# Kernel optimization log

Measured on AMD Instinct MI355X. Metric: run time of the kernel, lower is better.

The kernel has to match this reference:

```python
import jax, jax.numpy as jnp
import numpy as np

B, F_IN, NCH, T = 1, 1, 1536, 128
NW = [476, 476, 292]          # wires per plane (face 0)
NC = [10000, 10000, 10000]    # crossings per plane pair (01, 12, 20)
NCROSS = sum(NC)
E = 120000                    # ~4 nearest-neighbor edges per crossing node
N_FEAT_WIRE = 4
OUT_CH = 4
NODE_DIM = 2 * (F_IN + N_FEAT_WIRE) + 3  # = 13, matches GAT input dim


def setup_inputs() -> dict:
    key = jax.random.key(0)
    ks = jax.random.split(key, 18)
    x = jax.random.normal(ks[0], (B, F_IN, NCH, T), jnp.float32)
    chan_p0 = jax.random.randint(ks[1], (NW[0],), 0, NCH, jnp.int32)
    chan_p1 = jax.random.randint(ks[2], (NW[1],), 0, NCH, jnp.int32)
    chan_p2 = jax.random.randint(ks[3], (NW[2],), 0, NCH, jnp.int32)
    gidx_01 = jax.random.randint(ks[4], (NC[0], 2), 0, min(NW[0], NW[1]), jnp.int32)
    gidx_12 = jax.random.randint(ks[5], (NC[1], 2), 0, min(NW[1], NW[2]), jnp.int32)
    gidx_20 = jax.random.randint(ks[6], (NC[2], 2), 0, min(NW[2], NW[0]), jnp.int32)
    ray_01 = jax.random.normal(ks[7], (NC[0], 2), jnp.float32)
    ray_12 = jax.random.normal(ks[8], (NC[1], 2), jnp.float32)
    ray_20 = jax.random.normal(ks[9], (NC[2], 2), jnp.float32)
    edges = jax.random.randint(ks[10], (2, E), 0, NCROSS, jnp.int32)
    W_gat = jax.random.normal(ks[11], (NODE_DIM, OUT_CH), jnp.float32) * 0.1
    a_src = jax.random.normal(ks[12], (OUT_CH,), jnp.float32) * 0.1
    a_dst = jax.random.normal(ks[13], (OUT_CH,), jnp.float32) * 0.1
    b_gat = jnp.zeros((OUT_CH,), jnp.float32)
    W_mlp = jax.random.normal(ks[14], (OUT_CH, 1), jnp.float32) * 0.1
    b_mlp = jnp.zeros((1,), jnp.float32)
    return dict(x=x, chan_p0=chan_p0, chan_p1=chan_p1, chan_p2=chan_p2,
                gidx_01=gidx_01, gidx_12=gidx_12, gidx_20=gidx_20,
                ray_01=ray_01, ray_12=ray_12, ray_20=ray_20, edges=edges,
                W_gat=W_gat, a_src=a_src, a_dst=a_dst, b_gat=b_gat,
                W_mlp=W_mlp, b_mlp=b_mlp)


def _plane_feats(x, chan, plane_id):
    # x: [B,F,C,T] -> per-wire features [B,T,Nw,F+4]:
    # (signal, wire_ident, channel, 0, plane_id) -- mirrors as_wires_f0_pX.
    sig = jnp.transpose(x[:, :, chan, :], (0, 3, 2, 1))  # [B,T,Nw,F]
    nw = chan.shape[0]
    wire_id = jnp.arange(nw, dtype=jnp.float32)
    extra = jnp.stack([wire_id, chan.astype(jnp.float32),
                       jnp.zeros(nw, jnp.float32),
                       jnp.full((nw,), plane_id, jnp.float32)], axis=-1)  # [Nw,4]
    extra = jnp.broadcast_to(extra[None, None], sig.shape[:2] + extra.shape)
    return jnp.concatenate([sig, extra], axis=-1)


def _cross(fA, fB, gidx, rc):
    # crossing node features: wireA feats ++ wireB feats ++ ray xy ++ tick
    n = gidx.shape[0]
    tick = jnp.broadcast_to(jnp.arange(T, dtype=jnp.float32)[None, :, None, None],
                            (B, T, n, 1))
    rcb = jnp.broadcast_to(rc[None, None], (B, T, n, 2))
    return jnp.concatenate([fA[:, :, gidx[:, 0]], fB[:, :, gidx[:, 1]], rcb, tick],
                           axis=-1)  # [B,T,n,13]


def _gat_one(h, a_src, a_dst, src, dst):
    # single-graph, single-head GAT attention + aggregation. h: [N,OUT_CH]
    s = h @ a_src  # [N]
    d = h @ a_dst
    e = jax.nn.leaky_relu(s[src] + d[dst], 0.2)  # [E]
    m = jax.ops.segment_max(e, dst, num_segments=NCROSS)
    m = jnp.where(jnp.isfinite(m), m, 0.0)
    w = jnp.exp(e - m[dst])
    denom = jax.ops.segment_sum(w, dst, num_segments=NCROSS)
    msg = jax.ops.segment_sum(w[:, None] * h[src], dst, num_segments=NCROSS)
    return msg / (denom[:, None] + 1e-9)


def reference(x, chan_p0, chan_p1, chan_p2, gidx_01, gidx_12, gidx_20,
              ray_01, ray_12, ray_20, edges,
              W_gat, a_src, a_dst, b_gat, W_mlp, b_mlp):
    f0 = _plane_feats(x, chan_p0, 0.0)
    f1 = _plane_feats(x, chan_p1, 1.0)
    f2 = _plane_feats(x, chan_p2, 2.0)
    nodes = jnp.concatenate([_cross(f0, f1, gidx_01, ray_01),
                             _cross(f1, f2, gidx_12, ray_12),
                             _cross(f2, f0, gidx_20, ray_20)], axis=2)  # [B,T,N,13]
    h = nodes @ W_gat + b_gat  # [B,T,N,OUT_CH]
    src, dst = edges[0], edges[1]
    gat = jax.vmap(jax.vmap(lambda hh: _gat_one(hh, a_src, a_dst, src, dst)))
    g = gat(h)  # [B,T,N,OUT_CH]
    return jax.nn.sigmoid(g @ W_mlp + b_mlp)  # [B,T,N,1]
```

## Files before the change

### kernel.cpp

```cpp
#include <hip/hip_runtime.h>

#define T_TICKS 128
#define NCHAN   1536
#define NCPAIR  10000
#define NCROSS  30000
#define E_EDGES 120000
#define TG      8
#define NTG     (T_TICKS / TG)
#define NBLK_N  ((NCROSS + 255) / 256)
#define CAP     24
#define EPB     ((E_EDGES + NBLK_N - 1) / NBLK_N)


__global__ void k_feat(const float* __restrict__ x,
                       const int* __restrict__ c0, const int* __restrict__ c1,
                       const int* __restrict__ c2,
                       const int* __restrict__ g01, const int* __restrict__ g12,
                       const int* __restrict__ g20,
                       const float* __restrict__ r01,
                       const float* __restrict__ r12,
                       const float* __restrict__ r20,
                       const float* __restrict__ Wg,
                       const float* __restrict__ bg,
                       const float* __restrict__ as_,
                       const float* __restrict__ ad_,
                       const float* __restrict__ Wm,
                       const int* __restrict__ e_src,
                       const int* __restrict__ e_dst,
                       int* __restrict__ counts,
                       unsigned short* __restrict__ bucket,
                       float4* __restrict__ sp4, float4* __restrict__ dc4) {
    const int tid = threadIdx.x;
    const int tg = blockIdx.y;
    if (tg == 0) {
        const int lo = blockIdx.x * EPB;
        const int hi = min(lo + EPB, E_EDGES);
        for (int i = lo + tid; i < hi; i += 256) {
            const int s = e_src[i];
            const int d = e_dst[i];
            const int slot = atomicAdd(&counts[d], 1);
            if (slot < CAP) bucket[(size_t)d * CAP + slot] = (unsigned short)s;
        }
    }
    const int n = blockIdx.x * 256 + tid;
    if (n >= NCROSS) return;

    int iA, iB, m;
    float pA, pB;
    const int* cA;
    const int* cB;
    const float* ray;
    if (n < NCPAIR) {
        m = n; cA = c0; cB = c1; pA = 0.f; pB = 1.f; ray = r01;
        iA = g01[2 * m]; iB = g01[2 * m + 1];
    } else if (n < 2 * NCPAIR) {
        m = n - NCPAIR; cA = c1; cB = c2; pA = 1.f; pB = 2.f; ray = r12;
        iA = g12[2 * m]; iB = g12[2 * m + 1];
    } else {
        m = n - 2 * NCPAIR; cA = c2; cB = c0; pA = 2.f; pB = 0.f; ray = r20;
        iA = g20[2 * m]; iB = g20[2 * m + 1];
    }
    const int chA = cA[iA];
    const int chB = cB[iB];
    const float rx = ray[2 * m];
    const float ry = ray[2 * m + 1];

    float base[4];
#pragma unroll
    for (int c = 0; c < 4; c++) {
        base[c] = bg[c]
                + (float)iA  * Wg[1 * 4 + c] + (float)chA * Wg[2 * 4 + c]
                + pA         * Wg[4 * 4 + c]
                + (float)iB  * Wg[6 * 4 + c] + (float)chB * Wg[7 * 4 + c]
                + pB         * Wg[9 * 4 + c]
                + rx         * Wg[10 * 4 + c] + ry * Wg[11 * 4 + c];
    }
    float sB = 0, dB = 0, pBs = 0;
    float sA1 = 0, dA1 = 0, pA1 = 0;
    float sB1 = 0, dB1 = 0, pB1 = 0;
    float sT = 0, dT = 0, pT = 0;
#pragma unroll
    for (int c = 0; c < 4; c++) {
        const float va = as_[c], vd = ad_[c], vm = Wm[c];
        sB  += base[c] * va;  dB  += base[c] * vd;  pBs += base[c] * vm;
        sA1 += Wg[c] * va;    dA1 += Wg[c] * vd;    pA1 += Wg[c] * vm;
        sB1 += Wg[5*4+c]*va;  dB1 += Wg[5*4+c]*vd;  pB1 += Wg[5*4+c]*vm;
        sT  += Wg[12*4+c]*va; dT  += Wg[12*4+c]*vd; pT  += Wg[12*4+c]*vm;
    }
    if (tg == 0) {
        dc4[(size_t)n * 2]     = make_float4(dB, dA1, dB1, dT);
        dc4[(size_t)n * 2 + 1] = make_float4(__int_as_float(chA),
                                             __int_as_float(chB), 0.f, 0.f);
    }

    const int t0 = tg * TG;
    const float4 xa0 = *(const float4*)(x + chA * T_TICKS + t0);
    const float4 xa1 = *(const float4*)(x + chA * T_TICKS + t0 + 4);
    const float4 xb0 = *(const float4*)(x + chB * T_TICKS + t0);
    const float4 xb1 = *(const float4*)(x + chB * T_TICKS + t0 + 4);
    const float sa[8] = {xa0.x, xa0.y, xa0.z, xa0.w, xa1.x, xa1.y, xa1.z, xa1.w};
    const float sb[8] = {xb0.x, xb0.y, xb0.z, xb0.w, xb1.x, xb1.y, xb1.z, xb1.w};
    float sv[8], pv[8];
#pragma unroll
    for (int k = 0; k < TG; k++) {
        const float tk = (float)(t0 + k);
        sv[k] = sB  + sa[k] * sA1 + sb[k] * sB1 + tk * sT;
        pv[k] = pBs + sa[k] * pA1 + sb[k] * pB1 + tk * pT;
    }
    float4* rec = sp4 + ((size_t)tg * NCROSS + n) * 4;
    rec[0] = make_float4(sv[0], pv[0], sv[1], pv[1]);
    rec[1] = make_float4(sv[2], pv[2], sv[3], pv[3]);
    rec[2] = make_float4(sv[4], pv[4], sv[5], pv[5]);
    rec[3] = make_float4(sv[6], pv[6], sv[7], pv[7]);
}


__device__ __forceinline__ void upd(float& mx, float& den, float& p,
                                    const float e, const float pj) {
    const float dif = e - mx;
    const float ex = __expf(-fabsf(dif));
    const bool g = dif > 0.f;
    const float scale = g ? ex : 1.f;
    const float w = g ? 1.f : ex;
    mx = g ? e : mx;
    den = fmaf(den, scale, w);
    p = fmaf(p, scale, w * pj);
}

__global__ void k_gat(const float4* __restrict__ sp4,
                      const float4* __restrict__ dc4,
                      const float* __restrict__ x,
                      const int* __restrict__ counts,
                      const unsigned short* __restrict__ bucket,
                      const float* __restrict__ bm,
                      float* __restrict__ out) {
    const int lid = blockIdx.x;
    const int xcd = lid & 7;
    const int s   = lid >> 3;
    const int q   = s / NBLK_N;
    const int nb  = s - q * NBLK_N;
    const int tg  = xcd + 8 * q;
    const int t0  = tg * TG;
    const int bbase = nb * 256;
    const int tid = threadIdx.x;
    const int wsz = min(256, NCROSS - bbase);

    __shared__ int perm[256];
    __shared__ int bins[CAP + 1];
    __shared__ int boff[CAP + 1];
    __shared__ float lres[TG][257];

    int deg0 = 0;
    if (tid < wsz) deg0 = min(counts[bbase + tid], CAP);
    if (tid <= CAP) bins[tid] = 0;
    __syncthreads();
    int lp = 0;
    if (tid < wsz) lp = atomicAdd(&bins[deg0], 1);
    __syncthreads();
    if (tid == 0) {
        int run = 0;
        for (int d = CAP; d >= 0; d--) { boff[d] = run; run += bins[d]; }
    }
    __syncthreads();
    if (tid < wsz) perm[boff[deg0] + lp] = tid;
    __syncthreads();

    if (tid < wsz) {
        const int nloc = perm[tid];
        const int n = bbase + nloc;
        const int deg = min(counts[n], CAP);
        const unsigned short* bkt = bucket + (size_t)n * CAP;

        float dd[TG];
        {
            const float4 cd = dc4[(size_t)n * 2];
            const float4 cq = dc4[(size_t)n * 2 + 1];
            const int chA = __float_as_int(cq.x);
            const int chB = __float_as_int(cq.y);
            const float4 xa0 = *(const float4*)(x + chA * T_TICKS + t0);
            const float4 xa1 = *(const float4*)(x + chA * T_TICKS + t0 + 4);
            const float4 xb0 = *(const float4*)(x + chB * T_TICKS + t0);
            const float4 xb1 = *(const float4*)(x + chB * T_TICKS + t0 + 4);
            const float sa[8] = {xa0.x, xa0.y, xa0.z, xa0.w,
                                 xa1.x, xa1.y, xa1.z, xa1.w};
            const float sb[8] = {xb0.x, xb0.y, xb0.z, xb0.w,
                                 xb1.x, xb1.y, xb1.z, xb1.w};
            float dbase = fmaf((float)t0, cd.w, cd.x);
#pragma unroll
            for (int k = 0; k < TG; k++) {
                dd[k] = fmaf(sa[k], cd.y, fmaf(sb[k], cd.z, dbase));
                dbase += cd.w;
            }
        }

        float mx[TG], den[TG], pa[TG];
#pragma unroll
        for (int k = 0; k < TG; k++) { mx[k] = -INFINITY; den[k] = 0.f; pa[k] = 0.f; }

        const float4* spb = sp4 + (size_t)tg * NCROSS * 4;

        auto visit = [&](const float4 f0, const float4 f1,
                         const float4 f2, const float4 f3) {
            float e;
            e = f0.x + dd[0]; e = fmaxf(e, 0.2f * e); upd(mx[0], den[0], pa[0], e, f0.y);
            e = f0.z + dd[1]; e = fmaxf(e, 0.2f * e); upd(mx[1], den[1], pa[1], e, f0.w);
            e = f1.x + dd[2]; e = fmaxf(e, 0.2f * e); upd(mx[2], den[2], pa[2], e, f1.y);
            e = f1.z + dd[3]; e = fmaxf(e, 0.2f * e); upd(mx[3], den[3], pa[3], e, f1.w);
            e = f2.x + dd[4]; e = fmaxf(e, 0.2f * e); upd(mx[4], den[4], pa[4], e, f2.y);
            e = f2.z + dd[5]; e = fmaxf(e, 0.2f * e); upd(mx[5], den[5], pa[5], e, f2.w);
            e = f3.x + dd[6]; e = fmaxf(e, 0.2f * e); upd(mx[6], den[6], pa[6], e, f3.y);
            e = f3.z + dd[7]; e = fmaxf(e, 0.2f * e); upd(mx[7], den[7], pa[7], e, f3.w);
        };

        int j = 0;
        for (; j + 2 <= deg; j += 2) {
            const float4* r0 = spb + (size_t)bkt[j] * 4;
            const float4* r1 = spb + (size_t)bkt[j + 1] * 4;
            const float4 a0 = r0[0], a1 = r0[1], a2 = r0[2], a3 = r0[3];
            const float4 b0 = r1[0], b1 = r1[1], b2 = r1[2], b3 = r1[3];
            visit(a0, a1, a2, a3);
            visit(b0, b1, b2, b3);
        }
        if (j < deg) {
            const float4* r0 = spb + (size_t)bkt[j] * 4;
            visit(r0[0], r0[1], r0[2], r0[3]);
        }

        const float bb = bm[0];
#pragma unroll
        for (int k = 0; k < TG; k++) {
            const float logit = pa[k] / (den[k] + 1e-9f) + bb;
            lres[k][nloc] = 1.f / (1.f + __expf(-logit));
        }
    }
    __syncthreads();
    if (tid < wsz) {
#pragma unroll
        for (int k = 0; k < TG; k++) {
            out[(size_t)(t0 + k) * NCROSS + bbase + tid] = lres[k][tid];
        }
    }
}


extern "C" void kernel_launch(void* const* d_in, const int* in_sizes, int n_in,
                              void* d_out, int out_size, void* d_ws, size_t ws_size,
                              hipStream_t stream) {
    const float* x   = (const float*)d_in[0];
    const int* c0  = (const int*)d_in[1];
    const int* c1  = (const int*)d_in[2];
    const int* c2  = (const int*)d_in[3];
    const int* g01 = (const int*)d_in[4];
    const int* g12 = (const int*)d_in[5];
    const int* g20 = (const int*)d_in[6];
    const float* r01 = (const float*)d_in[7];
    const float* r12 = (const float*)d_in[8];
    const float* r20 = (const float*)d_in[9];
    const int* edges = (const int*)d_in[10];
    const float* Wg  = (const float*)d_in[11];
    const float* as_ = (const float*)d_in[12];
    const float* ad_ = (const float*)d_in[13];
    const float* bg  = (const float*)d_in[14];
    const float* Wm  = (const float*)d_in[15];
    const float* bm  = (const float*)d_in[16];
    float* out = (float*)d_out;

    const int* e_src = edges;
    const int* e_dst = edges + E_EDGES;

    char* ws = (char*)d_ws;
    size_t off = 0;
    int* counts            = (int*)(ws + off);            off += NCROSS * sizeof(int);
    off = (off + 63) & ~(size_t)63;
    unsigned short* bucket = (unsigned short*)(ws + off); off += (size_t)NCROSS * CAP * 2;
    off = (off + 63) & ~(size_t)63;
    float4* dc4            = (float4*)(ws + off);         off += (size_t)NCROSS * 32;
    off = (off + 255) & ~(size_t)255;
    float4* sp4            = (float4*)(ws + off);         off += (size_t)NTG * NCROSS * 64;
    (void)ws_size; (void)n_in; (void)in_sizes; (void)out_size;

    hipMemsetAsync(counts, 0, NCROSS * sizeof(int), stream);

    dim3 gridF(NBLK_N, NTG);
    k_feat<<<gridF, 256, 0, stream>>>(x, c0, c1, c2, g01, g12, g20,
                                      r01, r12, r20, Wg, bg, as_, ad_, Wm,
                                      e_src, e_dst, counts, bucket, sp4, dc4);
    k_gat<<<NBLK_N * NTG, 256, 0, stream>>>(sp4, dc4, x, counts, bucket, bm, out);
}
```

Before: 155.7 us.

## Split GAT aggregation across 8 lanes per node, one tick per lane

The GAT kernel now gives each node 8 threads, each handling one time tick, where before one thread processed all 8 ticks for its node. Blocks cover 32 nodes, and the grid becomes a 2D layout of node blocks by time groups, which drops the XCD-interleaved block index mapping. The goal is more parallelism and lower register pressure, so that latency of the irregular gathers is better hidden. In exchange each lane issues float2 loads instead of float4 rows, and the per-node edge-index and degree lookups are repeated across 8 lanes.

```diff
diff --git a/kernel.cpp b/kernel.cpp
--- a/kernel.cpp
+++ b/kernel.cpp
@@ -8,6 +8,8 @@
 #define TG      8
 #define NTG     (T_TICKS / TG)
 #define NBLK_N  ((NCROSS + 255) / 256)
+#define NODES_B 32
+#define NBLK_G  ((NCROSS + NODES_B - 1) / NODES_B)
 #define CAP     24
 #define EPB     ((E_EDGES + NBLK_N - 1) / NBLK_N)
 
@@ -127,118 +129,89 @@
     p = fmaf(p, scale, w * pj);
 }
 
-__global__ void k_gat(const float4* __restrict__ sp4,
+__global__ void k_gat(const float2* __restrict__ sp2,
                       const float4* __restrict__ dc4,
                       const float* __restrict__ x,
                       const int* __restrict__ counts,
                       const unsigned short* __restrict__ bucket,
                       const float* __restrict__ bm,
                       float* __restrict__ out) {
-    const int lid = blockIdx.x;
-    const int xcd = lid & 7;
-    const int s   = lid >> 3;
-    const int q   = s / NBLK_N;
-    const int nb  = s - q * NBLK_N;
-    const int tg  = xcd + 8 * q;
-    const int t0  = tg * TG;
-    const int bbase = nb * 256;
+    const int nb = blockIdx.x;
+    const int tg = blockIdx.y;
+    const int t0 = tg * TG;
+    const int bbase = nb * NODES_B;
     const int tid = threadIdx.x;
-    const int wsz = min(256, NCROSS - bbase);
-
-    __shared__ int perm[256];
+    const int wsz = min(NODES_B, NCROSS - bbase);
+    const int nsub = tid >> 3;
+    const int tk   = tid & 7;
+
+    __shared__ int perm[NODES_B];
     __shared__ int bins[CAP + 1];
     __shared__ int boff[CAP + 1];
-    __shared__ float lres[TG][257];
-
-    int deg0 = 0;
-    if (tid < wsz) deg0 = min(counts[bbase + tid], CAP);
+    __shared__ float lres[TG * 40];
+
     if (tid <= CAP) bins[tid] = 0;
     __syncthreads();
-    int lp = 0;
-    if (tid < wsz) lp = atomicAdd(&bins[deg0], 1);
+    int dg = 0, lp = 0;
+    if (tid < wsz) {
+        dg = min(counts[bbase + tid], CAP);
+        lp = atomicAdd(&bins[dg], 1);
+    }
     __syncthreads();
     if (tid == 0) {
         int run = 0;
         for (int d = CAP; d >= 0; d--) { boff[d] = run; run += bins[d]; }
     }
     __syncthreads();
-    if (tid < wsz) perm[boff[deg0] + lp] = tid;
-    __syncthreads();
-
-    if (tid < wsz) {
-        const int nloc = perm[tid];
+    if (tid < wsz) perm[boff[dg] + lp] = tid;
+    __syncthreads();
+
+    if (nsub < wsz) {
+        const int nloc = perm[nsub];
         const int n = bbase + nloc;
         const int deg = min(counts[n], CAP);
         const unsigned short* bkt = bucket + (size_t)n * CAP;
 
-        float dd[TG];
+        float dd;
         {
             const float4 cd = dc4[(size_t)n * 2];
             const float4 cq = dc4[(size_t)n * 2 + 1];
             const int chA = __float_as_int(cq.x);
             const int chB = __float_as_int(cq.y);
-            const float4 xa0 = *(const float4*)(x + chA * T_TICKS + t0);
-            const float4 xa1 = *(const float4*)(x + chA * T_TICKS + t0 + 4);
-            const float4 xb0 = *(const float4*)(x + chB * T_TICKS + t0);
-            const float4 xb1 = *(const float4*)(x + chB * T_TICKS + t0 + 4);
-            const float sa[8] = {xa0.x, xa0.y, xa0.z, xa0.w,
-                                 xa1.x, xa1.y, xa1.z, xa1.w};
-            const float sb[8] = {xb0.x, xb0.y, xb0.z, xb0.w,
-                                 xb1.x, xb1.y, xb1.z, xb1.w};
-            float dbase = fmaf((float)t0, cd.w, cd.x);
-#pragma unroll
-            for (int k = 0; k < TG; k++) {
-                dd[k] = fmaf(sa[k], cd.y, fmaf(sb[k], cd.z, dbase));
-                dbase += cd.w;
-            }
-        }
-
-        float mx[TG], den[TG], pa[TG];
-#pragma unroll
-        for (int k = 0; k < TG; k++) { mx[k] = -INFINITY; den[k] = 0.f; pa[k] = 0.f; }
-
-        const float4* spb = sp4 + (size_t)tg * NCROSS * 4;
-
-        auto visit = [&](const float4 f0, const float4 f1,
-                         const float4 f2, const float4 f3) {
-            float e;
-            e = f0.x + dd[0]; e = fmaxf(e, 0.2f * e); upd(mx[0], den[0], pa[0], e, f0.y);
-            e = f0.z + dd[1]; e = fmaxf(e, 0.2f * e); upd(mx[1], den[1], pa[1], e, f0.w);
-            e = f1.x + dd[2]; e = fmaxf(e, 0.2f * e); upd(mx[2], den[2], pa[2], e, f1.y);
-            e = f1.z + dd[3]; e = fmaxf(e, 0.2f * e); upd(mx[3], den[3], pa[3], e, f1.w);
-            e = f2.x + dd[4]; e = fmaxf(e, 0.2f * e); upd(mx[4], den[4], pa[4], e, f2.y);
-            e = f2.z + dd[5]; e = fmaxf(e, 0.2f * e); upd(mx[5], den[5], pa[5], e, f2.w);
-            e = f3.x + dd[6]; e = fmaxf(e, 0.2f * e); upd(mx[6], den[6], pa[6], e, f3.y);
-            e = f3.z + dd[7]; e = fmaxf(e, 0.2f * e); upd(mx[7], den[7], pa[7], e, f3.w);
-        };
+            const float xa = x[chA * T_TICKS + t0 + tk];
+            const float xb = x[chB * T_TICKS + t0 + tk];
+            dd = fmaf(xa, cd.y, fmaf(xb, cd.z, fmaf((float)(t0 + tk), cd.w, cd.x)));
+        }
+
+        float mx = -INFINITY, den = 0.f, pa = 0.f;
+        const float2* spb = sp2 + (size_t)tg * NCROSS * 8;
 
         int j = 0;
         for (; j + 2 <= deg; j += 2) {
-            const float4* r0 = spb + (size_t)bkt[j] * 4;
-            const float4* r1 = spb + (size_t)bkt[j + 1] * 4;
-            const float4 a0 = r0[0], a1 = r0[1], a2 = r0[2], a3 = r0[3];
-            const float4 b0 = r1[0], b1 = r1[1], b2 = r1[2], b3 = r1[3];
-            visit(a0, a1, a2, a3);
-            visit(b0, b1, b2, b3);
+            const int s0 = bkt[j];
+            const int s1 = bkt[j + 1];
+            const float2 f0 = spb[(size_t)s0 * 8 + tk];
+            const float2 f1 = spb[(size_t)s1 * 8 + tk];
+            float e0 = f0.x + dd; e0 = fmaxf(e0, 0.2f * e0);
+            upd(mx, den, pa, e0, f0.y);
+            float e1 = f1.x + dd; e1 = fmaxf(e1, 0.2f * e1);
+            upd(mx, den, pa, e1, f1.y);
         }
         if (j < deg) {
-            const float4* r0 = spb + (size_t)bkt[j] * 4;
-            visit(r0[0], r0[1], r0[2], r0[3]);
-        }
-
-        const float bb = bm[0];
-#pragma unroll
-        for (int k = 0; k < TG; k++) {
-            const float logit = pa[k] / (den[k] + 1e-9f) + bb;
-            lres[k][nloc] = 1.f / (1.f + __expf(-logit));
-        }
-    }
-    __syncthreads();
-    if (tid < wsz) {
-#pragma unroll
-        for (int k = 0; k < TG; k++) {
-            out[(size_t)(t0 + k) * NCROSS + bbase + tid] = lres[k][tid];
-        }
+            const float2 f0 = spb[(size_t)bkt[j] * 8 + tk];
+            float e0 = f0.x + dd; e0 = fmaxf(e0, 0.2f * e0);
+            upd(mx, den, pa, e0, f0.y);
+        }
+
+        const float logit = pa / (den + 1e-9f) + bm[0];
+        lres[tk * 40 + nloc] = 1.f / (1.f + __expf(-logit));
+    }
+    __syncthreads();
+    {
+        const int row = tid >> 5;
+        const int col = tid & 31;
+        if (col < wsz)
+            out[(size_t)(t0 + row) * NCROSS + bbase + col] = lres[row * 40 + col];
     }
 }
 
@@ -285,5 +258,7 @@
     k_feat<<<gridF, 256, 0, stream>>>(x, c0, c1, c2, g01, g12, g20,
                                       r01, r12, r20, Wg, bg, as_, ad_, Wm,
                                       e_src, e_dst, counts, bucket, sp4, dc4);
-    k_gat<<<NBLK_N * NTG, 256, 0, stream>>>(sp4, dc4, x, counts, bucket, bm, out);
-}
+    dim3 gridG(NBLK_G, NTG);
+    k_gat<<<gridG, 256, 0, stream>>>((const float2*)sp4, dc4, x, counts,
+                                     bucket, bm, out);
+}
```

Measured after the change: 159.1 us. +2.2%, slower.
